# Optimization experiments

Measured on AMD Instinct MI355X. Metric: run time of the kernel, lower is better.

The kernel has to match this reference:

```python
import jax, jax.numpy as jnp
import numpy as np

B = 2          # batch
S = 4096       # byte-level sequence length
D = 512        # d_hidden_bytelevel
BPL = 4        # bytes_per_latent
H = 16         # n_attention_heads
DQK = 64       # d_qkv_bytelevel (== rope d_hidden)
DLAT = 1024    # d_hidden_latent
LQ = S // BPL  # latent sequence length
EPS = 1.1920929e-07  # torch RMSNorm default eps = float32 finfo eps
ROPE_BASE = 10000.0


def _rope(x, pos):
    # x: [B, H, L, DQK], pos: [L] float positions. Half-split rotation.
    half = DQK // 2
    inv_freq = ROPE_BASE ** (-jnp.arange(half, dtype=jnp.float32) / half)  # [half]
    ang = pos[:, None] * inv_freq[None, :]                                 # [L, half]
    cos, sin = jnp.cos(ang), jnp.sin(ang)
    x1, x2 = x[..., :half], x[..., half:]
    return jnp.concatenate([x1 * cos - x2 * sin, x1 * sin + x2 * cos], axis=-1)


def setup_inputs() -> dict:
    key = jax.random.key(0)
    ks = jax.random.split(key, 9)
    s = 0.02
    return {
        "x": jax.random.normal(ks[0], (B, S, D), dtype=jnp.float32),
        "norm_w": jnp.ones((D,), dtype=jnp.float32),
        "wq_w": jax.random.normal(ks[1], (BPL * D, H * DQK), dtype=jnp.float32) * s,
        "wq_b": jax.random.normal(ks[2], (H * DQK,), dtype=jnp.float32) * s,
        "wkv_w": jax.random.normal(ks[3], (D, 2 * H * DQK), dtype=jnp.float32) * s,
        "wkv_b": jax.random.normal(ks[4], (2 * H * DQK,), dtype=jnp.float32) * s,
        "wout_w": jax.random.normal(ks[5], (H * DQK, DLAT), dtype=jnp.float32) * s,
        "wout_b": jax.random.normal(ks[6], (DLAT,), dtype=jnp.float32) * s,
        "wbyp_w": jax.random.normal(ks[7], (BPL * D, DLAT), dtype=jnp.float32) * s,
    }


def reference(x, norm_w, wq_w, wq_b, wkv_w, wkv_b, wout_w, wout_b, wbyp_w):
    # RMSNorm (elementwise affine)
    normalized = x * jax.lax.rsqrt(jnp.mean(x * x, axis=-1, keepdims=True) + EPS) * norm_w
    # merge groups of BPL bytes -> latent query tokens: [B, LQ, BPL*D]
    merged = normalized.reshape(B, LQ, BPL * D)
    # fused Q projection: [B, H, LQ, DQK]
    q = (merged @ wq_w + wq_b).reshape(B, LQ, H, DQK).transpose(0, 2, 1, 3)
    # merged KV projection: split dim first, then heads -> [B, S, 2, H, DQK]
    kv = (normalized @ wkv_w + wkv_b).reshape(B, S, 2, H, DQK)
    k = kv[:, :, 0].transpose(0, 2, 1, 3)  # [B, H, S, DQK]
    v = kv[:, :, 1].transpose(0, 2, 1, 3)
    # strided RoPE for Q (positions i*BPL), unit-stride for K
    q = _rope(q, jnp.arange(LQ, dtype=jnp.float32) * BPL)
    k = _rope(k, jnp.arange(S, dtype=jnp.float32))
    # SDPA (non-causal)
    scores = jnp.einsum('bhqd,bhkd->bhqk', q, k) * (1.0 / np.sqrt(DQK).astype(np.float32))
    attn = jax.nn.softmax(scores, axis=-1)
    attn_out = jnp.einsum('bhqk,bhkd->bhqd', attn, v)
    attn_concat = attn_out.transpose(0, 2, 1, 3).reshape(B, LQ, H * DQK)
    out = attn_concat @ wout_w + wout_b
    # bypass: raw x grouped by BPL, bias-free projection
    bypass = x.reshape(B, LQ, BPL * D) @ wbyp_w
    return out + bypass
```

## Files before the change

### kernel.cpp

```cpp
#include <hip/hip_runtime.h>

using u16 = unsigned short;
using u32 = unsigned int;

typedef __attribute__((ext_vector_type(8))) short bf16x8;
typedef __attribute__((ext_vector_type(8))) unsigned short u16x8;
typedef __attribute__((ext_vector_type(4))) float f32x4;
typedef __attribute__((ext_vector_type(16))) float f32x16;
typedef __attribute__((ext_vector_type(4))) u32 u32x4;

constexpr int Bb   = 2;
constexpr int Ss   = 4096;
constexpr int Dd   = 512;
constexpr int Hh   = 16;
constexpr int DQK  = 64;
constexpr int LQ   = 1024;
constexpr int DLAT = 1024;

#define QSCL 0.18033688011112042f

__device__ __forceinline__ u16 f2bf(float f){
  u32 u = __float_as_uint(f);
  u += 0x7FFFu + ((u >> 16) & 1u);
  return (u16)(u >> 16);
}
__device__ __forceinline__ u32 permpack(float hi, float lo){
  return __builtin_amdgcn_perm(__float_as_uint(hi), __float_as_uint(lo), 0x07060302u);
}

#define GLDS16(gp, lp) \
  __builtin_amdgcn_global_load_lds((const __attribute__((address_space(1))) u32*)(gp), \
                                   (__attribute__((address_space(3))) u32*)(lp), 16, 0, 0)

__global__ __launch_bounds__(256) void rmsnorm_kernel(
    const float* __restrict__ x, const float* __restrict__ w,
    u16* __restrict__ normb, u16* __restrict__ xb)
{
  const int lane = threadIdx.x & 63;
  const int row  = blockIdx.x * 4 + (threadIdx.x >> 6);
  const float4* xr = (const float4*)(x + (size_t)row * Dd);
  float4 a = xr[lane*2], b2 = xr[lane*2 + 1];
  float ss = a.x*a.x + a.y*a.y + a.z*a.z + a.w*a.w
           + b2.x*b2.x + b2.y*b2.y + b2.z*b2.z + b2.w*b2.w;
  #pragma unroll
  for (int off = 1; off < 64; off <<= 1) ss += __shfl_xor(ss, off);
  const float sc = rsqrtf(ss * (1.0f / Dd) + 1.1920929e-07f);
  const int c0 = lane * 8;
  const float4* wr4 = (const float4*)(w + c0);
  float4 w0 = wr4[0], w1 = wr4[1];
  u16x8 nv, xv;
  nv[0]=f2bf(a.x *sc*w0.x); nv[1]=f2bf(a.y *sc*w0.y); nv[2]=f2bf(a.z *sc*w0.z); nv[3]=f2bf(a.w *sc*w0.w);
  nv[4]=f2bf(b2.x*sc*w1.x); nv[5]=f2bf(b2.y*sc*w1.y); nv[6]=f2bf(b2.z*sc*w1.z); nv[7]=f2bf(b2.w*sc*w1.w);
  xv[0]=f2bf(a.x);  xv[1]=f2bf(a.y);  xv[2]=f2bf(a.z);  xv[3]=f2bf(a.w);
  xv[4]=f2bf(b2.x); xv[5]=f2bf(b2.y); xv[6]=f2bf(b2.z); xv[7]=f2bf(b2.w);
  *(u16x8*)(normb + (size_t)row * Dd + c0) = nv;
  *(u16x8*)(xb    + (size_t)row * Dd + c0) = xv;
}

__global__ __launch_bounds__(256) void rope_tab_kernel(float2* __restrict__ tab){
  int i = blockIdx.x * 256 + threadIdx.x;
  int pos = i >> 5, d = i & 31;
  float inv = exp2f(-(float)d * 0.41524101186092028f);
  float ang = (float)pos * inv;
  float s, c;
  sincosf(ang, &s, &c);
  tab[i] = make_float2(c, s);
}

__global__ __launch_bounds__(256) void transpose_cast_kernel(
    const float* __restrict__ W, u16* __restrict__ Wt,
    int N, int ldt, int koff)
{
  __shared__ float t[64][65];
  const int k0 = blockIdx.x * 64, n0 = blockIdx.y * 64;
  const int c = threadIdx.x & 63, r0 = threadIdx.x >> 6;
  #pragma unroll
  for (int i = 0; i < 16; ++i){
    int r = i*4 + r0;
    t[r][c] = W[(size_t)(k0 + r) * N + n0 + c];
  }
  __syncthreads();
  #pragma unroll
  for (int i = 0; i < 16; ++i){
    int r = i*4 + r0;
    Wt[(size_t)(n0 + r) * ldt + koff + k0 + c] = f2bf(t[c][r]);
  }
}

__device__ __forceinline__ void gemm_core64(
    const u16* __restrict__ A, int lda,
    const u16* __restrict__ Bt, int ldb, int kofs,
    int K, int bm0, int bn0, char* lds,
    f32x4 (&acc)[4])
{
  const int tid = threadIdx.x, lane = tid & 63, w = tid >> 6;
  const int l15 = lane & 15, l4 = lane >> 4;

  #pragma unroll
  for (int j = 0; j < 4; ++j) acc[j] = (f32x4){0.f, 0.f, 0.f, 0.f};

  auto stage = [&](int t){
    char* dst = lds + (t % 3) * 16384;
    const int k0 = t * 64;
    #pragma unroll
    for (int i = 0; i < 4; ++i){
      int u = i*256 + tid;
      int row = u >> 3;
      int colb = ((u & 7) * 16) ^ ((row & 7) << 4);
      const u16* src = (row < 64)
        ? A  + (size_t)(bm0 + row) * lda + k0 + (colb >> 1)
        : Bt + (size_t)(bn0 + row - 64) * ldb + kofs + k0 + (colb >> 1);
      GLDS16(src, dst + u*16);
    }
  };

  const int nt = K >> 6;
  stage(0);
  if (nt > 1) stage(1);

  #pragma unroll 1
  for (int t = 0; t < nt; ++t){
    if (t + 1 < nt) { asm volatile("s_waitcnt vmcnt(4)" ::: "memory"); }
    else            { asm volatile("s_waitcnt vmcnt(0)" ::: "memory"); }
    __builtin_amdgcn_sched_barrier(0);
    __builtin_amdgcn_s_barrier();

    const char* kb = lds + (t % 3) * 16384;
    bf16x8 af[2], bf[4][2];
    #pragma unroll
    for (int ks = 0; ks < 2; ++ks){
      const int row = w*16 + l15;
      af[ks] = *(const bf16x8*)(kb + row*128 + ((ks*64 + l4*16) ^ ((row & 7) << 4)));
    }
    #pragma unroll
    for (int j = 0; j < 4; ++j)
      #pragma unroll
      for (int ks = 0; ks < 2; ++ks){
        const int row = 64 + j*16 + l15;
        bf[j][ks] = *(const bf16x8*)(kb + row*128 + ((ks*64 + l4*16) ^ ((row & 7) << 4)));
      }
    asm volatile("s_waitcnt lgkmcnt(0)" ::: "memory");
    __builtin_amdgcn_sched_barrier(0);
    if (t + 2 < nt) stage(t + 2);

    __builtin_amdgcn_s_setprio(1);
    #pragma unroll
    for (int ks = 0; ks < 2; ++ks)
      #pragma unroll
      for (int j = 0; j < 4; ++j)
        acc[j] = __builtin_amdgcn_mfma_f32_16x16x32_bf16(af[ks], bf[j][ks], acc[j], 0, 0, 0);
    __builtin_amdgcn_s_setprio(0);
  }
}

__device__ __forceinline__ void gemm_core256(
    const u16* __restrict__ A, int lda, int ksplit,
    const u16* __restrict__ A2, int lda2,
    const u16* __restrict__ Bt, int ldb,
    int K, int bm0, int bn0, char* lds,
    f32x4 (&acc)[4][4])
{
  const int tid = threadIdx.x, lane = tid & 63, w = tid >> 6;
  const int wr = w >> 1, wc = w & 1;
  const int l15 = lane & 15, l4 = lane >> 4;

  #pragma unroll
  for (int i = 0; i < 4; ++i)
    #pragma unroll
    for (int j = 0; j < 4; ++j) acc[i][j] = (f32x4){0.f, 0.f, 0.f, 0.f};

  auto stage = [&](int t){
    char* dst = lds + (t % 3) * 49152;
    const int k0 = t * 64;
    #pragma unroll
    for (int i = 0; i < 6; ++i){
      int u = i*512 + tid;
      int row = u >> 3;
      int colb = ((u & 7) * 16) ^ ((row & 7) << 4);
      const u16* src;
      if (row < 256){
        if (k0 < ksplit) src = A  + (size_t)(bm0 + row) * lda  + k0 + (colb >> 1);
        else             src = A2 + (size_t)(bm0 + row) * lda2 + (k0 - ksplit) + (colb >> 1);
      } else {
        src = Bt + (size_t)(bn0 + row - 256) * ldb + k0 + (colb >> 1);
      }
      GLDS16(src, dst + u*16);
    }
  };

  const int nt = K >> 6;
  stage(0);
  if (nt > 1) stage(1);

  #pragma unroll 1
  for (int t = 0; t < nt; ++t){
    if (t + 1 < nt) { asm volatile("s_waitcnt vmcnt(6)" ::: "memory"); }
    else            { asm volatile("s_waitcnt vmcnt(0)" ::: "memory"); }
    __builtin_amdgcn_sched_barrier(0);
    __builtin_amdgcn_s_barrier();

    const char* kb = lds + (t % 3) * 49152;
    bf16x8 af[4][2], bf[4][2];
    #pragma unroll
    for (int i = 0; i < 4; ++i)
      #pragma unroll
      for (int ks = 0; ks < 2; ++ks){
        const int row = wr*64 + i*16 + l15;
        af[i][ks] = *(const bf16x8*)(kb + row*128 + ((ks*64 + l4*16) ^ ((row & 7) << 4)));
      }
    #pragma unroll
    for (int j = 0; j < 4; ++j)
      #pragma unroll
      for (int ks = 0; ks < 2; ++ks){
        const int row = 256 + wc*64 + j*16 + l15;
        bf[j][ks] = *(const bf16x8*)(kb + row*128 + ((ks*64 + l4*16) ^ ((row & 7) << 4)));
      }
    asm volatile("s_waitcnt lgkmcnt(0)" ::: "memory");
    __builtin_amdgcn_sched_barrier(0);
    if (t + 2 < nt) stage(t + 2);

    __builtin_amdgcn_s_setprio(1);
    #pragma unroll
    for (int ks = 0; ks < 2; ++ks)
      #pragma unroll
      for (int i = 0; i < 4; ++i)
        #pragma unroll
        for (int j = 0; j < 4; ++j)
          acc[i][j] = __builtin_amdgcn_mfma_f32_16x16x32_bf16(af[i][ks], bf[j][ks], acc[i][j], 0, 0, 0);
    __builtin_amdgcn_s_setprio(0);
  }
}

__global__ __launch_bounds__(512, 1) void qkv_kernel(
    const u16* __restrict__ normb,
    const u16* __restrict__ wtq, const u16* __restrict__ wtkv,
    const float* __restrict__ wq_b, const float* __restrict__ wkv_b,
    const float2* __restrict__ rtab,
    u16* __restrict__ Qb, u16* __restrict__ Kb, u16* __restrict__ Vtb)
{
  __shared__ char lds[147456];
  const int bid = blockIdx.x;
  const int lane = threadIdx.x & 63, w = threadIdx.x >> 6;
  const int wr = w >> 1, wc = w & 1;
  const int ml = (lane >> 4) * 4, nl = lane & 15;
  f32x4 acc[4][4];

  if (bid < 64){
    const int bm0 = (bid & 7) * 256, bn0 = (bid >> 3) * 128;
    gemm_core256(normb, 2048, 2048, normb, 2048, wtq, 2048, 2048, bm0, bn0, lds, acc);
    const int nbase = bn0 + wc*64;
    const int h = nbase >> 6;
    #pragma unroll
    for (int i = 0; i < 4; ++i){
      #pragma unroll
      for (int j = 0; j < 2; ++j){
        const int d1 = j*16 + nl;
        const float b1 = wq_b[nbase + j*16 + nl], b2v = wq_b[nbase + (j+2)*16 + nl];
        #pragma unroll
        for (int r = 0; r < 4; ++r){
          int m = bm0 + wr*64 + i*16 + ml + r;
          int b = m >> 10, lq = m & 1023;
          float x1 = acc[i][j][r] + b1;
          float x2 = acc[i][j+2][r] + b2v;
          float2 cs = rtab[(lq*4)*32 + d1];
          size_t ob = ((size_t)(b*Hh + h) * LQ + lq) * DQK;
          Qb[ob + d1]      = f2bf((x1*cs.x - x2*cs.y) * QSCL);
          Qb[ob + d1 + 32] = f2bf((x1*cs.y + x2*cs.x) * QSCL);
        }
      }
    }
  } else {
    const int t = bid - 64;
    const int bm0 = (t & 31) * 256, bn0 = (t >> 5) * 128;
    gemm_core256(normb, 512, 512, normb, 512, wtkv, 512, 512, bm0, bn0, lds, acc);
    const int nbase = bn0 + wc*64;
    const int kv = nbase >> 10;
    const int h = (nbase & 1023) >> 6;
    #pragma unroll
    for (int i = 0; i < 4; ++i){
      const int m0 = bm0 + wr*64 + i*16 + ml;
      const int b = m0 >> 12, s = m0 & 4095;
      if (kv == 0){
        #pragma unroll
        for (int r = 0; r < 4; ++r){
          size_t ob = ((size_t)(b*Hh + h) * Ss + s + r) * DQK;
          #pragma unroll
          for (int j = 0; j < 2; ++j){
            int d1 = j*16 + nl;
            float x1 = acc[i][j][r]   + wkv_b[nbase + j*16 + nl];
            float x2 = acc[i][j+2][r] + wkv_b[nbase + (j+2)*16 + nl];
            float2 cs = rtab[(s+r)*32 + d1];
            Kb[ob + d1]      = f2bf(x1*cs.x - x2*cs.y);
            Kb[ob + d1 + 32] = f2bf(x1*cs.y + x2*cs.x);
          }
        }
      } else {
        #pragma unroll
        for (int j = 0; j < 4; ++j){
          const int d = j*16 + nl;
          const float bb = wkv_b[nbase + d];
          uint2 pv;
          pv.x = permpack(acc[i][j][1] + bb, acc[i][j][0] + bb);
          pv.y = permpack(acc[i][j][3] + bb, acc[i][j][2] + bb);
          *(uint2*)(Vtb + (((size_t)(b*Hh + h)) * DQK + d) * Ss + s) = pv;
        }
      }
    }
  }
}

__global__ __launch_bounds__(256, 3) void out_kernel(
    const u16* __restrict__ ACb, const u16* __restrict__ xb,
    const u16* __restrict__ wto, const float* __restrict__ wout_b,
    float* __restrict__ outp)
{
  __shared__ char lds[49152];
  const int bm0 = blockIdx.x * 64, bn0 = blockIdx.y * 64;
  const int lane = threadIdx.x & 63, w = threadIdx.x >> 6;
  const int ml = (lane >> 4) * 4, nl = lane & 15;
  f32x4 acc[4], acc2[4];
  gemm_core64(ACb, 1024, wto, 3072, 0,    1024, bm0, bn0, lds, acc);
  __syncthreads();
  gemm_core64(xb,  2048, wto, 3072, 1024, 2048, bm0, bn0, lds, acc2);
  #pragma unroll
  for (int j = 0; j < 4; ++j){
    const int n = bn0 + j*16 + nl;
    const float bb = wout_b[n];
    #pragma unroll
    for (int r = 0; r < 4; ++r){
      int m = bm0 + w*16 + ml + r;
      outp[(size_t)m * DLAT + n] = acc[j][r] + acc2[j][r] + bb;
    }
  }
}

__global__ __launch_bounds__(512, 2) void flash_kernel(
    const u16* __restrict__ Qg, const u16* __restrict__ Kg,
    const u16* __restrict__ Vtg, float* __restrict__ Opart,
    float* __restrict__ lpart)
{
  const int tid = threadIdx.x, lane = tid & 63, w = tid >> 6;
  const int bid = blockIdx.x;
  const int swz = (bid & 7) * 32 + (bid >> 3);
  const int sq = swz & 3, qh = (swz >> 2) & 1, bh = swz >> 3;
  const int sbase = sq * 1024;
  const int l31 = lane & 31, hgl = lane >> 5;

  __shared__ char lds[49152];

  bf16x8 qf[2][4];
  #pragma unroll
  for (int qt = 0; qt < 2; ++qt)
    #pragma unroll
    for (int ks = 0; ks < 4; ++ks)
      qf[qt][ks] = *(const bf16x8*)(Qg + ((size_t)bh*LQ + qh*512 + w*64 + qt*32 + l31) * DQK + ks*16 + hgl*8);

  f32x16 o[2][2];
  #pragma unroll
  for (int qt = 0; qt < 2; ++qt)
    #pragma unroll
    for (int nd = 0; nd < 2; ++nd)
      #pragma unroll
      for (int r = 0; r < 16; ++r) o[qt][nd][r] = 0.f;
  float l_run[2] = {0.f, 0.f};

  auto stage = [&](int t){
    char* dst = lds + (t % 3) * 16384;
    const int s0 = sbase + t * 64;
    #pragma unroll
    for (int i = 0; i < 2; ++i){
      int u = (w*2 + i) * 64 + lane;
      int row = (u >> 3) & 63;
      int colb = ((u & 7) * 16) ^ ((row & 7) << 4);
      const u16* src = (u < 512)
          ? Kg  + ((size_t)bh*Ss  + s0 + row) * DQK + (colb >> 1)
          : Vtg + ((size_t)bh*DQK + row) * Ss + s0  + (colb >> 1);
      GLDS16(src, dst + u*16);
    }
  };

  stage(0);
  stage(1);

  #pragma unroll 1
  for (int t = 0; t < 16; ++t){
    if (t < 15) { asm volatile("s_waitcnt vmcnt(2)" ::: "memory"); }
    else        { asm volatile("s_waitcnt vmcnt(0)" ::: "memory"); }
    __builtin_amdgcn_sched_barrier(0);
    __builtin_amdgcn_s_barrier();

    const char* kb = lds + (t % 3) * 16384;
    bf16x8 kf[2][4], vf[2][4];
    #pragma unroll
    for (int kvt = 0; kvt < 2; ++kvt)
      #pragma unroll
      for (int ks = 0; ks < 4; ++ks){
        const int row = kvt*32 + l31;
        kf[kvt][ks] = *(const bf16x8*)(kb + row*128 + ((ks*32 + hgl*16) ^ ((row & 7) << 4)));
      }
    #pragma unroll
    for (int nd = 0; nd < 2; ++nd)
      #pragma unroll
      for (int k2 = 0; k2 < 4; ++k2){
        const int row = nd*32 + l31;
        vf[nd][k2] = *(const bf16x8*)(kb + 8192 + row*128 + ((k2*32 + hgl*16) ^ ((row & 7) << 4)));
      }
    asm volatile("s_waitcnt lgkmcnt(0)" ::: "memory");
    __builtin_amdgcn_sched_barrier(0);
    if (t < 14) stage(t + 2);

    #pragma unroll
    for (int qt = 0; qt < 2; ++qt){
      f32x16 sc[2];
      #pragma unroll
      for (int kvt = 0; kvt < 2; ++kvt)
        #pragma unroll
        for (int r = 0; r < 16; ++r) sc[kvt][r] = 0.f;
      __builtin_amdgcn_s_setprio(1);
      #pragma unroll
      for (int kvt = 0; kvt < 2; ++kvt)
        #pragma unroll
        for (int ks = 0; ks < 4; ++ks)
          sc[kvt] = __builtin_amdgcn_mfma_f32_32x32x16_bf16(kf[kvt][ks], qf[qt][ks], sc[kvt], 0, 0, 0);
      __builtin_amdgcn_s_setprio(0);

      float s_loc = 0.f;
      u32x4 paw[4];
      #pragma unroll
      for (int kvt = 0; kvt < 2; ++kvt){
        #pragma unroll
        for (int r = 0; r < 16; ++r){
          float p = __builtin_amdgcn_exp2f(sc[kvt][r]);
          sc[kvt][r] = p;
          s_loc += p;
        }
        #pragma unroll
        for (int k2r = 0; k2r < 2; ++k2r){
          u32 a0 = permpack(sc[kvt][k2r*8+1], sc[kvt][k2r*8+0]);
          u32 a1 = permpack(sc[kvt][k2r*8+3], sc[kvt][k2r*8+2]);
          u32 a2 = permpack(sc[kvt][k2r*8+5], sc[kvt][k2r*8+4]);
          u32 a3 = permpack(sc[kvt][k2r*8+7], sc[kvt][k2r*8+6]);
          asm("v_permlane32_swap_b32 %0, %1" : "+v"(a0), "+v"(a2));
          asm("v_permlane32_swap_b32 %0, %1" : "+v"(a1), "+v"(a3));
          const int k2 = kvt*2 + k2r;
          paw[k2][0] = a0; paw[k2][1] = a1;
          paw[k2][2] = a2; paw[k2][3] = a3;
        }
      }
      l_run[qt] += s_loc;

      __builtin_amdgcn_s_setprio(1);
      #pragma unroll
      for (int nd = 0; nd < 2; ++nd)
        #pragma unroll
        for (int k2 = 0; k2 < 4; ++k2)
          o[qt][nd] = __builtin_amdgcn_mfma_f32_32x32x16_bf16(
              __builtin_bit_cast(bf16x8, paw[k2]), vf[nd][k2], o[qt][nd], 0, 0, 0);
      __builtin_amdgcn_s_setprio(0);
    }
  }

  #pragma unroll
  for (int qt = 0; qt < 2; ++qt){
    float lf = l_run[qt] + __shfl_xor(l_run[qt], 32);
    float* Ob = Opart + ((size_t)sq * 32768 + (size_t)bh * 1024) * 64;
    #pragma unroll
    for (int nd = 0; nd < 2; ++nd)
      #pragma unroll
      for (int r = 0; r < 16; ++r){
        int q = qh*512 + w*64 + qt*32 + (r & 3) + 8*(r >> 2) + 4*hgl;
        Ob[(size_t)q * 64 + nd*32 + l31] = o[qt][nd][r];
      }
    if (hgl == 0)
      lpart[(size_t)sq * 32768 + (size_t)bh * 1024 + qh*512 + w*64 + qt*32 + l31] = lf;
  }
}

__global__ __launch_bounds__(256) void merge_kernel(
    const float* __restrict__ Opart, const float* __restrict__ lpart,
    u16* __restrict__ AC)
{
  int idx = blockIdx.x * 256 + threadIdx.x;
  int row = idx >> 3, dg = idx & 7;
  int bh = row >> 10, lq = row & 1023;
  int b = bh >> 4, h = bh & 15;
  float a[8];
  #pragma unroll
  for (int e = 0; e < 8; ++e) a[e] = 0.f;
  float lt = 0.f;
  #pragma unroll
  for (int p = 0; p < 4; ++p){
    const float4* pp = (const float4*)(Opart + ((size_t)p * 32768 + row) * 64 + dg * 8);
    float4 v0 = pp[0], v1 = pp[1];
    a[0]+=v0.x; a[1]+=v0.y; a[2]+=v0.z; a[3]+=v0.w;
    a[4]+=v1.x; a[5]+=v1.y; a[6]+=v1.z; a[7]+=v1.w;
    lt += lpart[(size_t)p * 32768 + row];
  }
  float rl = 1.0f / lt;
  u16x8 r;
  #pragma unroll
  for (int e = 0; e < 8; ++e) r[e] = f2bf(a[e] * rl);
  *(u16x8*)(AC + ((size_t)(b*LQ + lq)) * (Hh*DQK) + h*DQK + dg*8) = r;
}

extern "C" void kernel_launch(void* const* d_in, const int* in_sizes, int n_in,
                              void* d_out, int out_size, void* d_ws, size_t ws_size,
                              hipStream_t stream)
{
  (void)in_sizes; (void)n_in; (void)out_size; (void)ws_size;
  const float* x      = (const float*)d_in[0];
  const float* norm_w = (const float*)d_in[1];
  const float* wq_w   = (const float*)d_in[2];
  const float* wq_b   = (const float*)d_in[3];
  const float* wkv_w  = (const float*)d_in[4];
  const float* wkv_b  = (const float*)d_in[5];
  const float* wout_w = (const float*)d_in[6];
  const float* wout_b = (const float*)d_in[7];
  const float* wbyp_w = (const float*)d_in[8];
  float* outp = (float*)d_out;

  char* p = (char*)d_ws;
  u16* normb = (u16*)p; p += (size_t)8192*512*2;
  u16* xb    = (u16*)p; p += (size_t)8192*512*2;
  u16* wtq   = (u16*)p; p += (size_t)1024*2048*2;
  u16* wtkv  = (u16*)p; p += (size_t)2048*512*2;
  u16* wto   = (u16*)p; p += (size_t)1024*3072*2;
  u16* Qb    = (u16*)p; p += (size_t)32*1024*64*2;
  u16* Kb    = (u16*)p; p += (size_t)32*4096*64*2;
  u16* Vtb   = (u16*)p; p += (size_t)32*64*4096*2;
  u16* ACb   = (u16*)p; p += (size_t)2048*1024*2;
  float2* rtab = (float2*)p; p += (size_t)4096*32*sizeof(float2);
  float* Opart = (float*)p; p += (size_t)4*32768*64*4;
  float* lpart = (float*)p; p += (size_t)4*32768*4;

  rmsnorm_kernel<<<2048, 256, 0, stream>>>(x, norm_w, normb, xb);
  rope_tab_kernel<<<512, 256, 0, stream>>>(rtab);
  transpose_cast_kernel<<<dim3(32,16), 256, 0, stream>>>(wq_w,   wtq,  1024, 2048, 0);
  transpose_cast_kernel<<<dim3(8,32),  256, 0, stream>>>(wkv_w,  wtkv, 2048, 512,  0);
  transpose_cast_kernel<<<dim3(16,16), 256, 0, stream>>>(wout_w, wto,  1024, 3072, 0);
  transpose_cast_kernel<<<dim3(32,16), 256, 0, stream>>>(wbyp_w, wto,  1024, 3072, 1024);

  qkv_kernel<<<576, 512, 0, stream>>>(normb, wtq, wtkv, wq_b, wkv_b, rtab, Qb, Kb, Vtb);
  flash_kernel<<<256, 512, 0, stream>>>(Qb, Kb, Vtb, Opart, lpart);
  merge_kernel<<<1024, 256, 0, stream>>>(Opart, lpart, ACb);
  out_kernel<<<dim3(32,16), 256, 0, stream>>>(ACb, xb, wto, wout_b, outp);
}
```

Baseline: 131.1 us.

## Split flash KV into eight chunks, store partials in bf16, merge weight transposes

The flash attention kernel now splits the key/value sequence into eight 512-long chunks instead of four 1024-long ones, doubling the grid to 512 blocks to fill more compute units. Partial outputs are written as bf16 instead of fp32 to limit the extra partial traffic, and the merge kernel sums eight partials. The four weight transpose-cast launches are fused into one kernel to cut launch overhead. Storing partials in bf16 adds rounding error, and the extra chunks shorten each block's pipeline and add merge work.

```diff
diff --git a/kernel.cpp b/kernel.cpp
--- a/kernel.cpp
+++ b/kernel.cpp
@@ -67,12 +67,11 @@
   tab[i] = make_float2(c, s);
 }
 
-__global__ __launch_bounds__(256) void transpose_cast_kernel(
+__device__ __forceinline__ void tc_body(
     const float* __restrict__ W, u16* __restrict__ Wt,
-    int N, int ldt, int koff)
+    int N, int ldt, int koff, int k0, int n0)
 {
   __shared__ float t[64][65];
-  const int k0 = blockIdx.x * 64, n0 = blockIdx.y * 64;
   const int c = threadIdx.x & 63, r0 = threadIdx.x >> 6;
   #pragma unroll
   for (int i = 0; i < 16; ++i){
@@ -84,6 +83,26 @@
   for (int i = 0; i < 16; ++i){
     int r = i*4 + r0;
     Wt[(size_t)(n0 + r) * ldt + koff + k0 + c] = f2bf(t[c][r]);
+  }
+}
+
+__global__ __launch_bounds__(256) void transpose_all_kernel(
+    const float* __restrict__ wq_w, const float* __restrict__ wkv_w,
+    const float* __restrict__ wout_w, const float* __restrict__ wbyp_w,
+    u16* __restrict__ wtq, u16* __restrict__ wtkv, u16* __restrict__ wto)
+{
+  const int bid = blockIdx.x;
+  if (bid < 512){
+    tc_body(wq_w, wtq, 1024, 2048, 0, (bid & 31) * 64, (bid >> 5) * 64);
+  } else if (bid < 768){
+    int t = bid - 512;
+    tc_body(wkv_w, wtkv, 2048, 512, 0, (t & 7) * 64, (t >> 3) * 64);
+  } else if (bid < 1024){
+    int t = bid - 768;
+    tc_body(wout_w, wto, 1024, 3072, 0, (t & 15) * 64, (t >> 4) * 64);
+  } else {
+    int t = bid - 1024;
+    tc_body(wbyp_w, wto, 1024, 3072, 1024, (t & 31) * 64, (t >> 5) * 64);
   }
 }
 
@@ -336,14 +355,14 @@
 
 __global__ __launch_bounds__(512, 2) void flash_kernel(
     const u16* __restrict__ Qg, const u16* __restrict__ Kg,
-    const u16* __restrict__ Vtg, float* __restrict__ Opart,
+    const u16* __restrict__ Vtg, u16* __restrict__ Opart,
     float* __restrict__ lpart)
 {
   const int tid = threadIdx.x, lane = tid & 63, w = tid >> 6;
   const int bid = blockIdx.x;
-  const int swz = (bid & 7) * 32 + (bid >> 3);
-  const int sq = swz & 3, qh = (swz >> 2) & 1, bh = swz >> 3;
-  const int sbase = sq * 1024;
+  const int swz = (bid & 7) * 64 + (bid >> 3);
+  const int s8 = swz & 7, qh = (swz >> 3) & 1, bh = swz >> 4;
+  const int sbase = s8 * 512;
   const int l31 = lane & 31, hgl = lane >> 5;
 
   __shared__ char lds[49152];
@@ -383,9 +402,9 @@
   stage(1);
 
   #pragma unroll 1
-  for (int t = 0; t < 16; ++t){
-    if (t < 15) { asm volatile("s_waitcnt vmcnt(2)" ::: "memory"); }
-    else        { asm volatile("s_waitcnt vmcnt(0)" ::: "memory"); }
+  for (int t = 0; t < 8; ++t){
+    if (t < 7) { asm volatile("s_waitcnt vmcnt(2)" ::: "memory"); }
+    else       { asm volatile("s_waitcnt vmcnt(0)" ::: "memory"); }
     __builtin_amdgcn_sched_barrier(0);
     __builtin_amdgcn_s_barrier();
 
@@ -407,7 +426,7 @@
       }
     asm volatile("s_waitcnt lgkmcnt(0)" ::: "memory");
     __builtin_amdgcn_sched_barrier(0);
-    if (t < 14) stage(t + 2);
+    if (t < 6) stage(t + 2);
 
     #pragma unroll
     for (int qt = 0; qt < 2; ++qt){
@@ -463,21 +482,21 @@
   #pragma unroll
   for (int qt = 0; qt < 2; ++qt){
     float lf = l_run[qt] + __shfl_xor(l_run[qt], 32);
-    float* Ob = Opart + ((size_t)sq * 32768 + (size_t)bh * 1024) * 64;
+    u16* Ob = Opart + ((size_t)s8 * 32768 + (size_t)bh * 1024) * 64;
     #pragma unroll
     for (int nd = 0; nd < 2; ++nd)
       #pragma unroll
       for (int r = 0; r < 16; ++r){
         int q = qh*512 + w*64 + qt*32 + (r & 3) + 8*(r >> 2) + 4*hgl;
-        Ob[(size_t)q * 64 + nd*32 + l31] = o[qt][nd][r];
+        Ob[(size_t)q * 64 + nd*32 + l31] = f2bf(o[qt][nd][r]);
       }
     if (hgl == 0)
-      lpart[(size_t)sq * 32768 + (size_t)bh * 1024 + qh*512 + w*64 + qt*32 + l31] = lf;
+      lpart[(size_t)s8 * 32768 + (size_t)bh * 1024 + qh*512 + w*64 + qt*32 + l31] = lf;
   }
 }
 
 __global__ __launch_bounds__(256) void merge_kernel(
-    const float* __restrict__ Opart, const float* __restrict__ lpart,
+    const u16* __restrict__ Opart, const float* __restrict__ lpart,
     u16* __restrict__ AC)
 {
   int idx = blockIdx.x * 256 + threadIdx.x;
@@ -489,11 +508,11 @@
   for (int e = 0; e < 8; ++e) a[e] = 0.f;
   float lt = 0.f;
   #pragma unroll
-  for (int p = 0; p < 4; ++p){
-    const float4* pp = (const float4*)(Opart + ((size_t)p * 32768 + row) * 64 + dg * 8);
-    float4 v0 = pp[0], v1 = pp[1];
-    a[0]+=v0.x; a[1]+=v0.y; a[2]+=v0.z; a[3]+=v0.w;
-    a[4]+=v1.x; a[5]+=v1.y; a[6]+=v1.z; a[7]+=v1.w;
+  for (int p = 0; p < 8; ++p){
+    u16x8 v = *(const u16x8*)(Opart + ((size_t)p * 32768 + row) * 64 + dg * 8);
+    #pragma unroll
+    for (int e = 0; e < 8; ++e)
+      a[e] += __uint_as_float((u32)v[e] << 16);
     lt += lpart[(size_t)p * 32768 + row];
   }
   float rl = 1.0f / lt;
@@ -530,18 +549,15 @@
   u16* Vtb   = (u16*)p; p += (size_t)32*64*4096*2;
   u16* ACb   = (u16*)p; p += (size_t)2048*1024*2;
   float2* rtab = (float2*)p; p += (size_t)4096*32*sizeof(float2);
-  float* Opart = (float*)p; p += (size_t)4*32768*64*4;
-  float* lpart = (float*)p; p += (size_t)4*32768*4;
+  u16* Opart = (u16*)p; p += (size_t)8*32768*64*2;
+  float* lpart = (float*)p; p += (size_t)8*32768*4;
 
   rmsnorm_kernel<<<2048, 256, 0, stream>>>(x, norm_w, normb, xb);
   rope_tab_kernel<<<512, 256, 0, stream>>>(rtab);
-  transpose_cast_kernel<<<dim3(32,16), 256, 0, stream>>>(wq_w,   wtq,  1024, 2048, 0);
-  transpose_cast_kernel<<<dim3(8,32),  256, 0, stream>>>(wkv_w,  wtkv, 2048, 512,  0);
-  transpose_cast_kernel<<<dim3(16,16), 256, 0, stream>>>(wout_w, wto,  1024, 3072, 0);
-  transpose_cast_kernel<<<dim3(32,16), 256, 0, stream>>>(wbyp_w, wto,  1024, 3072, 1024);
+  transpose_all_kernel<<<1536, 256, 0, stream>>>(wq_w, wkv_w, wout_w, wbyp_w, wtq, wtkv, wto);
 
   qkv_kernel<<<576, 512, 0, stream>>>(normb, wtq, wtkv, wq_b, wkv_b, rtab, Qb, Kb, Vtb);
-  flash_kernel<<<256, 512, 0, stream>>>(Qb, Kb, Vtb, Opart, lpart);
+  flash_kernel<<<512, 512, 0, stream>>>(Qb, Kb, Vtb, Opart, lpart);
   merge_kernel<<<1024, 256, 0, stream>>>(Opart, lpart, ACb);
   out_kernel<<<dim3(32,16), 256, 0, stream>>>(ACb, xb, wto, wout_b, outp);
 }
```

New measurement: 128.3 us. -2.1%, faster.
